# Performance work log

Hardware: AMD Instinct MI355X
Metric: run time of the kernel (lower is better)

## Reference

```python
import jax, jax.numpy as jnp
import numpy as np
from jax import lax

N_NODES = 17
CONN = np.array([[15, 13], [13, 11], [16, 14], [14, 12], [11, 12], [5, 11], [6, 12],
                 [5, 6], [5, 7], [6, 8], [7, 9], [8, 10], [1, 2], [0, 1], [0, 2],
                 [1, 3], [2, 4], [3, 5], [4, 6]], dtype=np.int64)


def build_ahat():
    # PyG GCNConv norm: add self loops, deg = in-degree on target (col),
    # edge weight = deg^{-1/2}[src] * deg^{-1/2}[dst], aggregate src -> dst.
    src = np.concatenate([CONN[:, 0], np.arange(N_NODES)])
    dst = np.concatenate([CONN[:, 1], np.arange(N_NODES)])
    deg = np.zeros(N_NODES, dtype=np.float64)
    np.add.at(deg, dst, 1.0)
    dis = deg ** -0.5
    A = np.zeros((N_NODES, N_NODES), dtype=np.float64)
    np.add.at(A, (dst, src), dis[src] * dis[dst])
    return jnp.asarray(A, dtype=jnp.float32)

AHAT = build_ahat()  # (17, 17) normalized adjacency, directed as in source


def gcn_conv(h1, h2, W, b):
    # h1/h2: (B, T, 17, Cin). Only nodes 0..16 of the flattened cat(pose1, pose2)
    # batch -- i.e. pose1 sample 0 -- participate in message passing; all other
    # nodes only get their self-loop (weight 1) => plain linear.
    g1 = h1 @ W
    g2 = h2 @ W
    agg0 = jnp.einsum('ij,tjh->tih', AHAT, g1[0])  # (T, 17, H)
    g1 = g1.at[0].set(agg0)
    return g1 + b, g2 + b


def lstm_scan(x, Wih, Whh, bih, bhh, reverse=False):
    # x: (T, B, D). PyTorch gate order: i, f, g, o.
    B = x.shape[1]
    H = Whh.shape[1]
    xs = x[::-1] if reverse else x
    pre = xs @ Wih.T + (bih + bhh)  # (T, B, 4H), input part precomputed

    def step(carry, p):
        h, c = carry
        z = p + h @ Whh.T
        i, f, g, o = jnp.split(z, 4, axis=-1)
        c = jax.nn.sigmoid(f) * c + jax.nn.sigmoid(i) * jnp.tanh(g)
        h = jax.nn.sigmoid(o) * jnp.tanh(c)
        return (h, c), h

    init = (jnp.zeros((B, H), x.dtype), jnp.zeros((B, H), x.dtype))
    _, hs = lax.scan(step, init, pre)
    return hs[::-1] if reverse else hs  # time-ordered outputs (T, B, H)


def setup_inputs() -> dict:
    key = jax.random.key(0)
    ks = jax.random.split(key, 16)
    B, T, C_IN, H = 128, 256, 3, 128
    LH, NC = 256, 625
    D_LSTM = H * N_NODES  # 2176
    s = 0.05
    return {
        'pose1': jax.random.normal(ks[0], (B, T, N_NODES, C_IN), jnp.float32),
        'pose2': jax.random.normal(ks[1], (B, T, N_NODES, C_IN), jnp.float32),
        'W1': jax.random.normal(ks[2], (C_IN, H), jnp.float32) * s,
        'b1': jnp.zeros((H,), jnp.float32),
        'W2': jax.random.normal(ks[3], (H, H), jnp.float32) * s,
        'b2': jnp.zeros((H,), jnp.float32),
        'Wih_f': jax.random.normal(ks[4], (4 * LH, D_LSTM), jnp.float32) * s,
        'Whh_f': jax.random.normal(ks[5], (4 * LH, LH), jnp.float32) * s,
        'bih_f': jax.random.normal(ks[6], (4 * LH,), jnp.float32) * s,
        'bhh_f': jax.random.normal(ks[7], (4 * LH,), jnp.float32) * s,
        'Wih_b': jax.random.normal(ks[8], (4 * LH, D_LSTM), jnp.float32) * s,
        'Whh_b': jax.random.normal(ks[9], (4 * LH, LH), jnp.float32) * s,
        'bih_b': jax.random.normal(ks[10], (4 * LH,), jnp.float32) * s,
        'bhh_b': jax.random.normal(ks[11], (4 * LH,), jnp.float32) * s,
        'Wc': jax.random.normal(ks[12], (NC, 2 * LH), jnp.float32) * s,
        'bc': jnp.zeros((NC,), jnp.float32),
    }


def reference(pose1, pose2, W1, b1, W2, b2, Wih_f, Whh_f, bih_f, bhh_f,
              Wih_b, Whh_b, bih_b, bhh_b, Wc, bc):
    B, T = pose1.shape[:2]
    # GCN block (dropout is identity in eval mode)
    h1, h2 = gcn_conv(pose1, pose2, W1, b1)
    h1, h2 = jax.nn.relu(h1), jax.nn.relu(h2)
    h1, h2 = gcn_conv(h1, h2, W2, b2)
    # mean over the (pose1, pose2) pair, flatten node/channel dims
    feats = (0.5 * (h1 + h2)).reshape(B, T, -1)  # (B, T, 17*128)
    x = jnp.transpose(feats, (1, 0, 2))  # (T, B, D)
    hs_f = lstm_scan(x, Wih_f, Whh_f, bih_f, bhh_f, reverse=False)
    hs_b = lstm_scan(x, Wih_b, Whh_b, bih_b, bhh_b, reverse=True)
    last = jnp.concatenate([hs_f[-1], hs_b[-1]], axis=-1)  # (B, 512)
    feature_pool = jax.nn.relu(last)
    feature_cls = feature_pool @ Wc.T + bc
    return feature_pool, feature_cls
```

## Files before the change

### kernel.cpp

```cpp
#include <hip/hip_runtime.h>
#include <hip/hip_bf16.h>


#define TT 256
#define BB 128
#define NNODE 17
#define DD 2176
#define LHID 256
#define G4 1024
#define NCLS 625

typedef unsigned short u16t;

__device__ __constant__ int ESRC[19] = {15,13,16,14,11,5,6,5,5,6,7,8,1,0,0,1,2,3,4};
__device__ __constant__ int EDST[19] = {13,11,14,12,12,11,12,6,7,8,9,10,2,1,2,3,4,5,6};
__device__ __constant__ float DEGF[17] = {1,2,3,2,2,2,3,2,2,2,2,3,4,2,2,1,1};

__device__ inline float lo2f(unsigned u){ union{unsigned x; float f;} c; c.x = u << 16; return c.f; }
__device__ inline float hi2f(unsigned u){ union{unsigned x; float f;} c; c.x = u & 0xffff0000u; return c.f; }
__device__ inline u16t f2b(float f){
    __hip_bfloat16 h = __float2bfloat16(f);
    u16t s; __builtin_memcpy(&s, &h, 2); return s;
}
__device__ inline float b2f(u16t s){ union{unsigned x; float f;} c; c.x = ((unsigned)s) << 16; return c.f; }
__device__ inline unsigned pack2(float a, float b){
    return (unsigned)f2b(a) | ((unsigned)f2b(b) << 16);
}
__device__ inline float fsig(float x){ return __fdividef(1.f, 1.f + __expf(-x)); }
__device__ inline float ftanh(float x){ float e = __expf(2.f*x); return 1.f - __fdividef(2.f, e + 1.f); }
__device__ inline float sigm(float x){ return 1.f / (1.f + expf(-x)); }

typedef __attribute__((ext_vector_type(8))) short bf16x8;
typedef __attribute__((ext_vector_type(4))) float f32x4;
typedef __attribute__((ext_vector_type(4))) unsigned u32x4;

__device__ inline bf16x8 asB(u32x4 v){ bf16x8 r; __builtin_memcpy(&r, &v, 16); return r; }

__device__ inline void gload16(const void* g, void* l){
    __builtin_amdgcn_global_load_lds(
        (const __attribute__((address_space(1))) void*)g,
        (__attribute__((address_space(3))) void*)l, 16, 0, 0);
}

__global__ void k_w2t(const float* __restrict__ W2, __hip_bfloat16* __restrict__ W2Tb){
    int g = blockIdx.x * 256 + threadIdx.x;
    int k = g >> 7, n = g & 127;
    W2Tb[n * 128 + k] = __float2bfloat16(W2[g]);
}

__global__ void k_wfrag(const float* __restrict__ Whh, __hip_bfloat16* __restrict__ WTfrag){
    int g = blockIdx.x * 256 + threadIdx.x;
    int f = g >> 6, lane = g & 63;
    int w = f >> 5, kc = (f >> 2) & 7, nt = f & 3;
    int col = nt*256 + w*16 + (lane & 15);
    int k0  = kc*32 + (lane >> 4)*8;
    const float* src = Whh + (size_t)col * 256 + k0;
    float4 f0 = *(const float4*)src;
    float4 f1 = *(const float4*)(src + 4);
    uint4 o;
    o.x = pack2(f0.x, f0.y); o.y = pack2(f0.z, f0.w);
    o.z = pack2(f1.x, f1.y); o.w = pack2(f1.z, f1.w);
    *(uint4*)((char*)WTfrag + (size_t)g * 16) = o;
}

__global__ __launch_bounds__(512) void k_gcnfused(
    const float* __restrict__ pose1, const float* __restrict__ pose2,
    const float* __restrict__ W1, const float* __restrict__ b1,
    const float* __restrict__ b2, const __hip_bfloat16* __restrict__ W2Tb,
    __hip_bfloat16* __restrict__ feats)
{
    __shared__ u16t  Abuf[272][136];
    __shared__ u16t  BsmT[128][136];
    __shared__ float ps4[2][16][17][4];
    __shared__ float araw[17*128];
    __shared__ float araw2[17*128];
    __shared__ float As[289];

    const int tid = threadIdx.x;
    const int blk = blockIdx.x;
    const int t   = blk >> 3;
    const int bc  = blk & 7;

    for (int idx = tid; idx < 1632; idx += 512){
        int p_ = idx >= 816 ? 1 : 0;
        int r  = idx - p_ * 816;
        int bl = r / 51, i = r - bl * 51;
        int n = i / 3, c = i - n * 3;
        const float* src = p_ ? pose2 : pose1;
        ps4[p_][bl][n][c] = src[(size_t)((bc*16 + bl) * TT + t) * 51 + i];
    }
    {
        const uint4* src = (const uint4*)W2Tb;
        for (int r = 0; r < 2; ++r){
            int f0 = (tid + r * 512) * 16;
            int n = f0 >> 7, k0 = f0 & 127;
            uint4 v0 = src[(tid + r*512)*2 + 0];
            uint4 v1 = src[(tid + r*512)*2 + 1];
            *(uint4*)&BsmT[n][k0]     = v0;
            *(uint4*)&BsmT[n][k0 + 8] = v1;
        }
    }
    if (bc == 0 && tid < 289){
        int i = tid / 17, j = tid - (tid/17)*17;
        float a = (i == j) ? 1.0f / DEGF[i] : 0.0f;
        for (int e = 0; e < 19; ++e)
            if (EDST[e] == i && ESRC[e] == j)
                a += 1.0f / sqrtf(DEGF[i] * DEGF[j]);
        As[tid] = a;
    }

    const int h = tid & 127;
    const int q = tid >> 7;
    const float w10 = W1[h], w11 = W1[128 + h], w12 = W1[256 + h];
    const float b1h = b1[h];
    __syncthreads();

    float a2st[5];
    int nl[5], nv = 0;
    for (int s = 0; s < 5; ++s){ int n = q + 4*s; if (n < NNODE) nl[nv++] = n; }
    for (int s = 0; s < nv; ++s){
        int n = nl[s];
        for (int bl = 0; bl < 16; ++bl){
            float4 p1 = *(const float4*)&ps4[0][bl][n][0];
            float4 p2 = *(const float4*)&ps4[1][bl][n][0];
            float a1 = p1.x*w10 + p1.y*w11 + p1.z*w12;
            float a2 = p2.x*w10 + p2.y*w11 + p2.z*w12;
            if (bc == 0 && bl == 0){
                araw[n*128 + h] = a1;
                a2st[s] = a2;
            } else {
                float r1 = fmaxf(a1 + b1h, 0.f);
                float r2 = fmaxf(a2 + b1h, 0.f);
                Abuf[n*16 + bl][h] = f2b(0.5f*(r1 + r2));
            }
        }
    }
    __syncthreads();
    if (bc == 0){
        for (int s = 0; s < nv; ++s){
            int n = nl[s]; float a = 0.f;
            #pragma unroll
            for (int j = 0; j < NNODE; ++j) a += As[n*17 + j] * araw[j*128 + h];
            araw2[n*128 + h] = fmaxf(a + b1h, 0.f);
        }
    }
    __syncthreads();
    if (bc == 0){
        for (int s = 0; s < nv; ++s){
            int n = nl[s]; float a = 0.f;
            #pragma unroll
            for (int j = 0; j < NNODE; ++j) a += As[n*17 + j] * araw2[j*128 + h];
            float r2 = fmaxf(a2st[s] + b1h, 0.f);
            Abuf[n*16 + 0][h] = f2b(0.5f*(a + r2));
        }
    }
    __syncthreads();

    const int w = tid >> 6, l = tid & 63;
    const int l15 = l & 15, q8 = (l >> 4) * 8, q4 = (l >> 4) * 4;
    float bias[8];
    #pragma unroll
    for (int nt = 0; nt < 8; ++nt) bias[nt] = b2[nt*16 + l15];

    bf16x8 Bf[4][8];
    #pragma unroll
    for (int kc = 0; kc < 4; ++kc)
        #pragma unroll
        for (int nt = 0; nt < 8; ++nt)
            Bf[kc][nt] = *(const bf16x8*)&BsmT[nt*16 + l15][kc*32 + q8];

    u16t* Cb = (u16t*)feats;
    for (int mt = w; mt < NNODE; mt += 8){
        f32x4 acc[8];
        #pragma unroll
        for (int nt = 0; nt < 8; ++nt) acc[nt] = (f32x4){0.f,0.f,0.f,0.f};
        #pragma unroll
        for (int kc = 0; kc < 4; ++kc){
            bf16x8 a = *(const bf16x8*)&Abuf[mt*16 + l15][kc*32 + q8];
            #pragma unroll
            for (int nt = 0; nt < 8; ++nt)
                acc[nt] = __builtin_amdgcn_mfma_f32_16x16x32_bf16(a, Bf[kc][nt], acc[nt], 0,0,0);
        }
        #pragma unroll
        for (int nt = 0; nt < 8; ++nt)
            #pragma unroll
            for (int r = 0; r < 4; ++r){
                size_t row = (size_t)(blk*16 + q4 + r) * NNODE + mt;
                Cb[row*128 + nt*16 + l15] = f2b(acc[nt][r] + bias[nt]);
            }
    }
}

__global__ __launch_bounds__(256) void k_gemm_mfma(
    const __hip_bfloat16* __restrict__ A, const float* __restrict__ Bw,
    const float* __restrict__ bi1, const float* __restrict__ bi2,
    u16t* __restrict__ pre2)
{
    __shared__ u16t Asm[128][32];
    __shared__ u16t Bsm[128][32];
    const int tid = threadIdx.x;
    const int w = tid >> 6;
    const int l = tid & 63;

    const int blk = blockIdx.x;
    const int xcd = blk & 7;
    const int i_  = blk >> 3;
    const int bx  = xcd * 32 + (i_ >> 3);
    const int by  = i_ & 7;

    const size_t m0 = (size_t)bx * 128;
    const int n0 = by * 128;
    const int mw = (w >> 1) * 64;
    const int nw = (w & 1) * 64;

    f32x4 acc[4][4];
    #pragma unroll
    for (int s = 0; s < 4; ++s)
        #pragma unroll
        for (int t_ = 0; t_ < 4; ++t_)
            acc[s][t_] = (f32x4){0.f, 0.f, 0.f, 0.f};

    const u16t* Ab = (const u16t*)A;
    const int arow = w*32 + (l>>2);
    const int akoff = (l&3)*8;
    const int brow = w*32 + (l>>1);
    const int bko  = (l&1)*16;
    const int fr = l & 15, fq = (l >> 4) * 8;

    for (int kt = 0; kt < DD; kt += 32){
        gload16(Ab + (m0 + arow)*DD + kt + akoff,      &Asm[arow][akoff]);
        gload16(Ab + (m0 + arow + 16)*DD + kt + akoff, &Asm[arow+16][akoff]);
        const float* bp = Bw + (size_t)(n0 + brow)*DD + kt + bko;
        float4 f0 = *(const float4*)bp;
        float4 f1 = *(const float4*)(bp+4);
        float4 f2 = *(const float4*)(bp+8);
        float4 f3 = *(const float4*)(bp+12);
        uint4 o0, o1;
        o0.x = pack2(f0.x,f0.y); o0.y = pack2(f0.z,f0.w);
        o0.z = pack2(f1.x,f1.y); o0.w = pack2(f1.z,f1.w);
        o1.x = pack2(f2.x,f2.y); o1.y = pack2(f2.z,f2.w);
        o1.z = pack2(f3.x,f3.y); o1.w = pack2(f3.z,f3.w);
        *(uint4*)&Bsm[brow][bko]   = o0;
        *(uint4*)&Bsm[brow][bko+8] = o1;
        __syncthreads();

        bf16x8 af[4], bf[4];
        #pragma unroll
        for (int s = 0; s < 4; ++s) af[s] = *(const bf16x8*)&Asm[mw + s*16 + fr][fq];
        #pragma unroll
        for (int t_ = 0; t_ < 4; ++t_) bf[t_] = *(const bf16x8*)&Bsm[nw + t_*16 + fr][fq];
        #pragma unroll
        for (int s = 0; s < 4; ++s)
            #pragma unroll
            for (int t_ = 0; t_ < 4; ++t_)
                acc[s][t_] = __builtin_amdgcn_mfma_f32_16x16x32_bf16(af[s], bf[t_], acc[s][t_], 0, 0, 0);
        __syncthreads();
    }

    const int cr = (l >> 4) * 4;
    const int cc = l & 15;
    const int tIdx = bx;
    #pragma unroll
    for (int t_ = 0; t_ < 4; ++t_){
        int col = n0 + nw + t_*16 + cc;
        float bias = bi1[col] + bi2[col];
        int gate = col >> 8;
        int j    = col & 255;
        size_t cbase = (size_t)tIdx*131072 + (size_t)(j>>4)*1024 + (size_t)(j&15)*4 + gate;
        #pragma unroll
        for (int s = 0; s < 4; ++s)
            #pragma unroll
            for (int r = 0; r < 4; ++r){
                int b = mw + s*16 + cr + r;
                pre2[cbase + (size_t)(b>>4)*16384 + ((b&15)>>2)*256 + (b&3)*64]
                    = f2b(acc[s][t_][r] + bias);
            }
    }
}

__global__ __launch_bounds__(256) void k_lstm_b(
    const __hip_bfloat16* __restrict__ feats255,
    const float* __restrict__ Wih_b,
    const float* __restrict__ bih_b, const float* __restrict__ bhh_b,
    float* __restrict__ h_b)
{
    __shared__ float fs[DD];
    const int tid = threadIdx.x;
    const int b = blockIdx.x;
    const unsigned* fbu = (const unsigned*)(feats255 + (size_t)b * DD);
    for (int i = tid; i < DD/2; i += 256){
        unsigned u = fbu[i];
        fs[2*i] = lo2f(u); fs[2*i+1] = hi2f(u);
    }
    __syncthreads();

    const int w = tid >> 6, lane = tid & 63;
    const int j = blockIdx.y * 4 + w;
    const float* Wi = Wih_b + (size_t)j * DD;
    const float* Wg = Wih_b + (size_t)(512 + j) * DD;
    const float* Wo = Wih_b + (size_t)(768 + j) * DD;
    float si = 0.f, sg = 0.f, so = 0.f;
    #pragma unroll 2
    for (int i = 0; i < 34; ++i){
        int k = lane + i*64;
        float f = fs[k];
        si += f * Wi[k]; sg += f * Wg[k]; so += f * Wo[k];
    }
    #pragma unroll
    for (int off = 32; off > 0; off >>= 1){
        si += __shfl_down(si, off);
        sg += __shfl_down(sg, off);
        so += __shfl_down(so, off);
    }
    if (lane == 0){
        float zi = si + bih_b[j]       + bhh_b[j];
        float zg = sg + bih_b[512 + j] + bhh_b[512 + j];
        float zo = so + bih_b[768 + j] + bhh_b[768 + j];
        float c = sigm(zi) * tanhf(zg);
        h_b[(size_t)b*LHID + j] = sigm(zo) * tanhf(c);
    }
}

__global__ __launch_bounds__(1024, 4) void k_lstm_f11(
    const u16t* __restrict__ pre2,
    const __hip_bfloat16* __restrict__ WTfrag,
    float* __restrict__ hout)
{
    __shared__ u16t Wl[65536];
    __shared__ __align__(16) float zbuf[256][4];
    __shared__ __align__(16) u16t hbuf[256];

    const int tid = threadIdx.x;
    const int w = tid >> 6, l = tid & 63;
    const int q = l >> 4, l15 = l & 15, q8 = q * 8;
    const int g = blockIdx.x;
    const u16t* wtf = (const u16t*)WTfrag;

    {
        const uint4* srcq = (const uint4*)wtf;
        uint4* dstq = (uint4*)Wl;
        for (int i = tid; i < 8192; i += 1024){
            int iw = i >> 9, fi = (i >> 6) & 7, il = i & 63;
            dstq[i] = srcq[(iw*32 + 24 + fi)*64 + il];
        }
    }
    if (tid < 256) hbuf[tid] = 0;

    u32x4 Bv[6][4];
    #pragma unroll
    for (int kc = 0; kc < 6; ++kc)
        #pragma unroll
        for (int nt = 0; nt < 4; ++nt){
            Bv[kc][nt] = *(const u32x4*)(wtf + (((size_t)(w*32 + kc*4 + nt))*64 + l)*8);
            asm volatile("" : "+v"(Bv[kc][nt]));
        }

    const int j = tid;
    float cst = 0.f;
    const size_t pj = (size_t)(g >> 4)*16384 + (size_t)((g & 15) >> 2)*256
                    + (size_t)(g & 3)*64 + (size_t)(j >> 4)*1024 + (size_t)(j & 15)*4;
    const u16t* pp = pre2 + pj;
    union { uint2 v; u16t s4[4]; } prc, prn;
    if (tid < 256) prc.v = *(const uint2*)pp;
    __syncthreads();

    #pragma unroll 1
    for (int t = 0; t < TT; ++t){
        if (tid < 256){
            int tn = (t + 1 < TT) ? t + 1 : t;
            prn.v = *(const uint2*)(pp + (size_t)tn*131072);
        }

        f32x4 acc[4];
        #pragma unroll
        for (int nt = 0; nt < 4; ++nt) acc[nt] = (f32x4){0.f,0.f,0.f,0.f};

        #pragma unroll
        for (int kc = 6; kc < 8; ++kc){
            bf16x8 ah = *(const bf16x8*)&hbuf[kc*32 + q8];
            #pragma unroll
            for (int nt = 0; nt < 4; ++nt){
                bf16x8 bL = *(const bf16x8*)&Wl[((w*8 + (kc-6)*4 + nt)*64 + l)*8];
                acc[nt] = __builtin_amdgcn_mfma_f32_16x16x32_bf16(ah, bL, acc[nt], 0,0,0);
            }
        }
        #pragma unroll
        for (int kc = 0; kc < 6; ++kc){
            bf16x8 ah = *(const bf16x8*)&hbuf[kc*32 + q8];
            #pragma unroll
            for (int nt = 0; nt < 4; ++nt)
                acc[nt] = __builtin_amdgcn_mfma_f32_16x16x32_bf16(ah, asB(Bv[kc][nt]), acc[nt], 0,0,0);
        }

        if (q == 0){
            float4 zq;
            zq.x = acc[0][0]; zq.y = acc[1][0]; zq.z = acc[2][0]; zq.w = acc[3][0];
            *(float4*)&zbuf[w*16 + l15][0] = zq;
        }
        __syncthreads();

        if (tid < 256){
            float4 z = *(const float4*)&zbuf[j][0];
            float zi = z.x + b2f(prc.s4[0]);
            float zf = z.y + b2f(prc.s4[1]);
            float zg = z.z + b2f(prc.s4[2]);
            float zo = z.w + b2f(prc.s4[3]);
            float cn = fsig(zf)*cst + fsig(zi)*ftanh(zg);
            cst = cn;
            float hh = fsig(zo)*ftanh(cn);
            if (t < TT - 1)
                hbuf[j] = f2b(hh);
            else
                hout[(size_t)g*LHID + j] = hh;
        }
        prc = prn;
        __syncthreads();
    }
}

__global__ __launch_bounds__(256) void k_head(
    const float* __restrict__ h_f, const float* __restrict__ h_b,
    const float* __restrict__ Wc, const float* __restrict__ bc,
    float* __restrict__ out)
{
    __shared__ float pool[512];
    const int b = blockIdx.x, tid = threadIdx.x;
    float p0 = fmaxf(h_f[(size_t)b*LHID + tid], 0.f);
    float p1 = fmaxf(h_b[(size_t)b*LHID + tid], 0.f);
    pool[tid] = p0; pool[256 + tid] = p1;
    out[(size_t)b*512 + tid]       = p0;
    out[(size_t)b*512 + 256 + tid] = p1;
    __syncthreads();
    for (int n = tid; n < NCLS; n += 256){
        float a = bc[n];
        const float* ww = Wc + (size_t)n * 512;
        #pragma unroll 4
        for (int k = 0; k < 512; k += 4){
            float4 wv = *(const float4*)(ww + k);
            a += pool[k]*wv.x + pool[k+1]*wv.y + pool[k+2]*wv.z + pool[k+3]*wv.w;
        }
        out[(size_t)BB*512 + (size_t)b*NCLS + n] = a;
    }
}

extern "C" void kernel_launch(void* const* d_in, const int* in_sizes, int n_in,
                              void* d_out, int out_size, void* d_ws, size_t ws_size,
                              hipStream_t stream) {
    const float* pose1 = (const float*)d_in[0];
    const float* pose2 = (const float*)d_in[1];
    const float* W1    = (const float*)d_in[2];
    const float* b1    = (const float*)d_in[3];
    const float* W2    = (const float*)d_in[4];
    const float* b2    = (const float*)d_in[5];
    const float* Wih_f = (const float*)d_in[6];
    const float* Whh_f = (const float*)d_in[7];
    const float* bih_f = (const float*)d_in[8];
    const float* bhh_f = (const float*)d_in[9];
    const float* Wih_b = (const float*)d_in[10];
    const float* bih_b = (const float*)d_in[12];
    const float* bhh_b = (const float*)d_in[13];
    const float* Wc    = (const float*)d_in[14];
    const float* bc    = (const float*)d_in[15];
    (void)in_sizes; (void)n_in; (void)out_size; (void)ws_size;
    float* out = (float*)d_out;
    char* ws = (char*)d_ws;

    __hip_bfloat16* WTfrag = (__hip_bfloat16*)(ws + 0);
    __hip_bfloat16* W2Tb   = (__hip_bfloat16*)(ws + 524288);
    float*          h_b    = (float*)(ws + 557056);
    float*          h_f    = (float*)(ws + 688128);
    __hip_bfloat16* feats  = (__hip_bfloat16*)(ws + 2097152);
    u16t*           pre2   = (u16t*)(ws + 144703488);

    k_w2t     <<<64, 256, 0, stream>>>(W2, W2Tb);
    k_wfrag   <<<128, 256, 0, stream>>>(Whh_f, WTfrag);
    k_gcnfused<<<2048, 512, 0, stream>>>(pose1, pose2, W1, b1, b2, W2Tb, feats);
    k_gemm_mfma<<<2048, 256, 0, stream>>>(feats, Wih_f, bih_f, bhh_f, pre2);
    k_lstm_b  <<<dim3(128, 64), 256, 0, stream>>>(feats + (size_t)255*BB*DD, Wih_b, bih_b, bhh_b, h_b);
    k_lstm_f11<<<128, 1024, 0, stream>>>(pre2, WTfrag, h_f);
    k_head    <<<128, 256, 0, stream>>>(h_f, h_b, Wc, bc, out);
}
```

Baseline: 1.110 ms.

## Apply LSTM gates in MFMA lanes with double-buffered hidden state, one barrier per step

The forward LSTM recurrence kernel now applies the gate nonlinearities directly in the MFMA-owning lanes (q==0), so the zbuf round trip through shared memory and its barrier go away. The hidden state is double-buffered (hA[2][256]), so the single remaining __syncthreads per timestep covers the read/write hazard. This cuts one of two block-wide barriers per serial step. The trade-off is that the gate math now runs scattered across 16 waves (16 lanes each) instead of 4 dense waves, and the launch-bounds attribute is switched to an explicit waves_per_eu setting.

```diff
diff --git a/kernel.cpp b/kernel.cpp
--- a/kernel.cpp
+++ b/kernel.cpp
@@ -321,14 +321,14 @@
     }
 }
 
-__global__ __launch_bounds__(1024, 4) void k_lstm_f11(
+__global__ __attribute__((amdgpu_flat_work_group_size(1024,1024), amdgpu_waves_per_eu(4,4)))
+void k_lstm_f12(
     const u16t* __restrict__ pre2,
     const __hip_bfloat16* __restrict__ WTfrag,
     float* __restrict__ hout)
 {
     __shared__ u16t Wl[65536];
-    __shared__ __align__(16) float zbuf[256][4];
-    __shared__ __align__(16) u16t hbuf[256];
+    __shared__ __align__(16) u16t hA[2][256];
 
     const int tid = threadIdx.x;
     const int w = tid >> 6, l = tid & 63;
@@ -344,7 +344,7 @@
             dstq[i] = srcq[(iw*32 + 24 + fi)*64 + il];
         }
     }
-    if (tid < 256) hbuf[tid] = 0;
+    if (tid < 512) ((u16t*)hA)[tid] = 0;
 
     u32x4 Bv[6][4];
     #pragma unroll
@@ -355,18 +355,21 @@
             asm volatile("" : "+v"(Bv[kc][nt]));
         }
 
-    const int j = tid;
+    const int j = w*16 + l15;
     float cst = 0.f;
     const size_t pj = (size_t)(g >> 4)*16384 + (size_t)((g & 15) >> 2)*256
-                    + (size_t)(g & 3)*64 + (size_t)(j >> 4)*1024 + (size_t)(j & 15)*4;
+                    + (size_t)(g & 3)*64 + (size_t)w*1024 + (size_t)l15*4;
     const u16t* pp = pre2 + pj;
     union { uint2 v; u16t s4[4]; } prc, prn;
-    if (tid < 256) prc.v = *(const uint2*)pp;
+    prc.v = make_uint2(0u, 0u);
+    if (q == 0) prc.v = *(const uint2*)pp;
     __syncthreads();
 
     #pragma unroll 1
     for (int t = 0; t < TT; ++t){
-        if (tid < 256){
+        const int tb = t & 1, nxt = tb ^ 1;
+
+        if (q == 0){
             int tn = (t + 1 < TT) ? t + 1 : t;
             prn.v = *(const uint2*)(pp + (size_t)tn*131072);
         }
@@ -377,7 +380,7 @@
 
         #pragma unroll
         for (int kc = 6; kc < 8; ++kc){
-            bf16x8 ah = *(const bf16x8*)&hbuf[kc*32 + q8];
+            bf16x8 ah = *(const bf16x8*)&hA[tb][kc*32 + q8];
             #pragma unroll
             for (int nt = 0; nt < 4; ++nt){
                 bf16x8 bL = *(const bf16x8*)&Wl[((w*8 + (kc-6)*4 + nt)*64 + l)*8];
@@ -386,30 +389,22 @@
         }
         #pragma unroll
         for (int kc = 0; kc < 6; ++kc){
-            bf16x8 ah = *(const bf16x8*)&hbuf[kc*32 + q8];
+            bf16x8 ah = *(const bf16x8*)&hA[tb][kc*32 + q8];
             #pragma unroll
             for (int nt = 0; nt < 4; ++nt)
                 acc[nt] = __builtin_amdgcn_mfma_f32_16x16x32_bf16(ah, asB(Bv[kc][nt]), acc[nt], 0,0,0);
         }
 
         if (q == 0){
-            float4 zq;
-            zq.x = acc[0][0]; zq.y = acc[1][0]; zq.z = acc[2][0]; zq.w = acc[3][0];
-            *(float4*)&zbuf[w*16 + l15][0] = zq;
-        }
-        __syncthreads();
-
-        if (tid < 256){
-            float4 z = *(const float4*)&zbuf[j][0];
-            float zi = z.x + b2f(prc.s4[0]);
-            float zf = z.y + b2f(prc.s4[1]);
-            float zg = z.z + b2f(prc.s4[2]);
-            float zo = z.w + b2f(prc.s4[3]);
+            float zi = acc[0][0] + b2f(prc.s4[0]);
+            float zf = acc[1][0] + b2f(prc.s4[1]);
+            float zg = acc[2][0] + b2f(prc.s4[2]);
+            float zo = acc[3][0] + b2f(prc.s4[3]);
             float cn = fsig(zf)*cst + fsig(zi)*ftanh(zg);
             cst = cn;
             float hh = fsig(zo)*ftanh(cn);
             if (t < TT - 1)
-                hbuf[j] = f2b(hh);
+                hA[nxt][j] = f2b(hh);
             else
                 hout[(size_t)g*LHID + j] = hh;
         }
@@ -477,6 +472,6 @@
     k_gcnfused<<<2048, 512, 0, stream>>>(pose1, pose2, W1, b1, b2, W2Tb, feats);
     k_gemm_mfma<<<2048, 256, 0, stream>>>(feats, Wih_f, bih_f, bhh_f, pre2);
     k_lstm_b  <<<dim3(128, 64), 256, 0, stream>>>(feats + (size_t)255*BB*DD, Wih_b, bih_b, bhh_b, h_b);
-    k_lstm_f11<<<128, 1024, 0, stream>>>(pre2, WTfrag, h_f);
+    k_lstm_f12<<<128, 1024, 0, stream>>>(pre2, WTfrag, h_f);
     k_head    <<<128, 256, 0, stream>>>(h_f, h_b, Wc, bc, out);
 }
```

Result: slower. 1.181 ms (+6.3%).
